# Optimization experiments

Hardware: AMD Instinct MI355X
Metric: run time of the kernel (lower is better)

The kernel has to match this reference:

```python
import jax, jax.numpy as jnp
import numpy as np

DIM = 512
HEADS = 8
DIM_HEAD = 64
INNER = HEADS * DIM_HEAD  # 512
PATCH = 64
M = 3
IN_CH = PATCH * PATCH // 2      # 2048
OUT_CH = IN_CH // 2             # 1024
B, N = 8, PATCH * PATCH // 4    # 8, 1024
SCALE = DIM_HEAD ** -0.5


def setup_inputs() -> dict:
    key = jax.random.key(0)
    ks = jax.random.split(key, 16)
    rn = lambda k, shp, s: (jax.random.normal(k, shp, dtype=jnp.float32) * s)
    inp = rn(ks[0], (B, N, DIM), 1.0)
    x = rn(ks[1], (B, N, DIM), 1.0)
    y = rn(ks[2], (B, N, DIM), 1.0)
    # Linear params (torch convention: W [out, in], y = x @ W.T + b)
    Wq = rn(ks[3], (INNER, DIM), DIM ** -0.5)
    bq = jnp.zeros((INNER,), jnp.float32)
    Wkv = rn(ks[4], (2 * INNER, DIM), DIM ** -0.5)
    bkv = jnp.zeros((2 * INNER,), jnp.float32)
    Wf = rn(ks[5], (OUT_CH + M, IN_CH + M), (IN_CH + M) ** -0.5)
    bf = jnp.zeros((OUT_CH + M,), jnp.float32)
    Wo = rn(ks[6], (DIM, INNER), INNER ** -0.5)
    bo = jnp.zeros((DIM,), jnp.float32)
    # memory tokens (xavier_normal std = sqrt(2/(m+inner)))
    std = np.sqrt(2.0 / (M + INNER))
    m_k = rn(ks[7], (1, M, INNER), std)
    m_v = rn(ks[8], (1, M, INNER), std)
    Sm_k = rn(ks[9], (1, M, INNER), std)
    Sm_v = rn(ks[10], (1, M, INNER), std)
    return dict(inp=inp, x=x, y=y, Wq=Wq, bq=bq, Wkv=Wkv, bkv=bkv,
                Wf=Wf, bf=bf, Wo=Wo, bo=bo,
                m_k=m_k, m_v=m_v, Sm_k=Sm_k, Sm_v=Sm_v)


def _split_heads(t):
    # 'b n (h d) -> b h n d'
    b, n, _ = t.shape
    return t.reshape(b, n, HEADS, DIM_HEAD).transpose(0, 2, 1, 3)


def _mem_view(p, b):
    # torch: p.expand(b, M, INNER).view(b, HEADS, M, DIM_HEAD) — raw reshape
    return jnp.broadcast_to(p, (b, M, INNER)).reshape(b, HEADS, M, DIM_HEAD)


def reference(inp, x, y, Wq, bq, Wkv, bkv, Wf, bf, Wo, bo, m_k, m_v, Sm_k, Sm_v):
    b = inp.shape[0]
    context = jnp.concatenate([x, y], axis=1)            # [b, 2n, dim]
    q = _split_heads(inp @ Wq.T + bq)                    # [b, h, n, d]
    kv = context @ Wkv.T + bkv
    k, v = jnp.split(kv, 2, axis=-1)
    k, v = _split_heads(k), _split_heads(v)              # [b, h, 2n, d]
    mk = np.sqrt(DIM_HEAD).astype(np.float32) * _mem_view(m_k, b)
    mv = np.sqrt(M).astype(np.float32) * _mem_view(m_v, b)
    k = jnp.concatenate([k, mk], axis=2)                 # [b, h, 2n+m, d]
    v = jnp.concatenate([v, mv], axis=2)
    dots = jnp.einsum('bhid,bhjd->bhij', q, k) * SCALE
    cross_attn = jax.nn.softmax(dots, axis=-1)           # [b, h, n, 2n+m]

    skv = inp @ Wkv.T + bkv
    S_k, S_v = jnp.split(skv, 2, axis=-1)
    S_k, S_v = _split_heads(S_k), _split_heads(S_v)      # [b, h, n, d]
    Smk = np.sqrt(DIM_HEAD).astype(np.float32) * _mem_view(Sm_k, b)
    Smv = np.sqrt(M).astype(np.float32) * _mem_view(Sm_v, b)
    Sk = jnp.concatenate([S_k, Smk], axis=2)             # [b, h, n+m, d]
    Sv = jnp.concatenate([S_v, Smv], axis=2)
    dots2 = jnp.einsum('bhid,bhjd->bhij', q, Sk) * SCALE
    self_attn = jax.nn.softmax(dots2, axis=-1)           # [b, h, n, n+m]

    cross_attn = cross_attn @ Wf.T + bf                  # [b, h, n, n+m]
    attn = cross_attn + self_attn
    out = jnp.einsum('bhij,bhjd->bhid', attn, Sv)        # [b, h, n, d]
    out = out.transpose(0, 2, 1, 3).reshape(b, -1, INNER)
    return out @ Wo.T + bo                               # [b, n, dim]
```

## Files before the change

### kernel.cpp

```cpp
#include <hip/hip_runtime.h>
#include <hip/hip_bf16.h>
#include <type_traits>

using bf16 = __hip_bfloat16;
typedef float f32x4 __attribute__((ext_vector_type(4)));
typedef __bf16 bf16x8_t __attribute__((ext_vector_type(8)));
typedef short  s16x8_t  __attribute__((ext_vector_type(8)));

template <typename V, typename = void> struct MfmaWorks : std::false_type {};
template <typename V>
struct MfmaWorks<V, std::void_t<decltype(__builtin_amdgcn_mfma_f32_16x16x32_bf16(
    std::declval<V>(), std::declval<V>(), std::declval<f32x4>(), 0, 0, 0))>> : std::true_type {};
using frag_t = std::conditional_t<MfmaWorks<bf16x8_t>::value, bf16x8_t, s16x8_t>;

template <typename V>
__device__ __forceinline__ f32x4 mfma_16x16x32(V a, V b, f32x4 c) {
    return __builtin_amdgcn_mfma_f32_16x16x32_bf16(a, b, c, 0, 0, 0);
}

__device__ __forceinline__ void gld_lds16(const void* g, void* l) {
    __builtin_amdgcn_global_load_lds(
        (const __attribute__((address_space(1))) unsigned int*)g,
        (__attribute__((address_space(3))) unsigned int*)l, 16, 0, 0);
}

__device__ __forceinline__ float ldin(const void* p, long i, int f32) {
    return f32 ? ((const float*)p)[i] : __bfloat162float(((const bf16*)p)[i]);
}

__global__ void detect_dtype(const void* __restrict__ inp, int* __restrict__ flag)
{
    const int t = threadIdx.x;
    int sane_cnt = 0;
#pragma unroll
    for (int s = 0; s < 4; s++) {
        float v = __bfloat162float(((const bf16*)inp)[2 * (t + 64 * s)]);
        float a = fabsf(v);
        bool sane = (a == 0.f) || (a > 9e-4f && a < 1000.f);
        unsigned long long m = __ballot(sane);
        sane_cnt += (int)__popcll(m);
    }
    if (t == 0) *flag = (sane_cnt > 128) ? 0 : 1;
}

__global__ __launch_bounds__(256)
void cvt_gen8(const void* __restrict__ src, long srcOff, bf16* __restrict__ dst,
              long nsrc, long ndst, const int* __restrict__ flag, float scale)
{
    const int f = *flag;
    const long i0 = ((long)blockIdx.x * 256 + threadIdx.x) * 8;
    if (i0 >= ndst) return;
#pragma unroll
    for (int u = 0; u < 8; u++) {
        const long i = i0 + u;
        if (i < ndst) dst[i] = __float2bfloat16(i < nsrc ? scale * ldin(src, srcOff + i, f) : 0.f);
    }
}

__global__ __launch_bounds__(256)
void cvt_weights(const void* __restrict__ Wq, const void* __restrict__ Wkv,
                 const void* __restrict__ Wo,
                 bf16* __restrict__ WqB, bf16* __restrict__ WkvB, bf16* __restrict__ WoB,
                 const int* __restrict__ flag, float qscale)
{
    const int f = *flag;
    long id = (long)blockIdx.x * 256 + threadIdx.x;
    const void* src; bf16* dst; float sc;
    if (blockIdx.x < 128)      { src = Wq;  dst = WqB;  sc = qscale; }
    else if (blockIdx.x < 384) { src = Wkv; dst = WkvB; sc = 1.f; id -= 128L * 256; }
    else                       { src = Wo;  dst = WoB;  sc = 1.f; id -= 384L * 256; }
    const long i0 = id * 8;
#pragma unroll
    for (int u = 0; u < 8; u++)
        dst[i0 + u] = __float2bfloat16(sc * ldin(src, i0 + u, f));
}

__global__ __launch_bounds__(256)
void cvt_small(const void* __restrict__ bq, const void* __restrict__ bkv,
               const void* __restrict__ bo, const void* __restrict__ mk,
               const void* __restrict__ Smk, const void* __restrict__ Smv,
               bf16* __restrict__ bqB, bf16* __restrict__ bkvB, bf16* __restrict__ boB,
               bf16* __restrict__ mkS, bf16* __restrict__ SmkS, bf16* __restrict__ SmvS,
               const int* __restrict__ flag, float qscale)
{
    const int f = *flag;
    const void* src; bf16* dst; int n; float sc;
    switch (blockIdx.x) {
        case 0:  src = bq;  dst = bqB;  n = 512;  sc = qscale;     break;
        case 1:  src = bkv; dst = bkvB; n = 1024; sc = 1.f;        break;
        case 2:  src = bo;  dst = boB;  n = 512;  sc = 1.f;        break;
        case 3:  src = mk;  dst = mkS;  n = 1536; sc = 8.f;        break;
        case 4:  src = Smk; dst = SmkS; n = 1536; sc = 8.f;        break;
        default: src = Smv; dst = SmvS; n = 1536; sc = 1.7320508f; break;
    }
    for (int i = threadIdx.x; i < n; i += 256)
        dst[i] = __float2bfloat16(sc * ldin(src, i, f));
}

__global__ __launch_bounds__(256)
void cvt_ctx8(const void* __restrict__ x, const void* __restrict__ y,
              bf16* __restrict__ ctx, const int* __restrict__ flag)
{
    const int f = *flag;
    const long i0 = ((long)blockIdx.x * 256 + threadIdx.x) * 8;
    const long r = i0 >> 9, c0 = i0 & 511;
    const long b = r >> 11, jj = r & 2047;
    const void* src = (jj < 1024) ? x : y;
    const long  soff = (jj < 1024) ? ((b * 1024 + jj) * 512 + c0)
                                   : ((b * 1024 + (jj - 1024)) * 512 + c0);
#pragma unroll
    for (int u = 0; u < 8; u++)
        ctx[i0 + u] = __float2bfloat16(ldin(src, soff + u, f));
}

__global__ __launch_bounds__(256)
void cvt_wft(const void* __restrict__ Wf, const void* __restrict__ bff,
             bf16* __restrict__ WfT, const int* __restrict__ flag)
{
    const int f = *flag;
    const long i0 = ((long)blockIdx.x * 256 + threadIdx.x) * 8;
    if (i0 >= 2176L * 1056) return;
    const long j = i0 / 1056, r0 = i0 % 1056;
    __align__(16) bf16 tmp[8];
#pragma unroll
    for (int u = 0; u < 8; u++) {
        const long r = r0 + u;
        float v = 0.f;
        if (r < 1027) {
            if (j < 2051)       v = ldin(Wf, r * 2051 + j, f);
            else if (j == 2051) v = ldin(bff, r, f);
        }
        tmp[u] = __float2bfloat16(v);
    }
    *(uint4*)(WfT + i0) = *(const uint4*)tmp;
}

__global__ __launch_bounds__(256)
void pack_k(const bf16* __restrict__ Ck, const bf16* __restrict__ mkS, bf16* __restrict__ kb)
{
    const long id = (long)blockIdx.x * 256 + threadIdx.x;
    const long bh = id / (2176 * 8);
    const long rem = id % (2176 * 8);
    const long j = rem >> 3;
    const long dg = (rem & 7) << 3;
    const long b = bh >> 3, h = bh & 7;
    bf16* dst = kb + (bh * 2176 + j) * 64 + dg;
    if (j < 2048) {
        *(uint4*)dst = *(const uint4*)(Ck + (b * 2048 + j) * 512 + h * 64 + dg);
    } else if (j < 2051) {
        *(uint4*)dst = *(const uint4*)(mkS + h * 192 + (j - 2048) * 64 + dg);
    } else {
        uint4 zz = {0, 0, 0, 0};
        *(uint4*)dst = zz;
    }
}

__global__ __launch_bounds__(256)
void pack_sk(const bf16* __restrict__ Cskv, const bf16* __restrict__ SmkS, bf16* __restrict__ Skb)
{
    const long id = (long)blockIdx.x * 256 + threadIdx.x;
    const long bh = id / (1152 * 8);
    const long rem = id % (1152 * 8);
    const long j = rem >> 3;
    const long dg = (rem & 7) << 3;
    const long b = bh >> 3, h = bh & 7;
    bf16* dst = Skb + (bh * 1152 + j) * 64 + dg;
    if (j < 1024) {
        *(uint4*)dst = *(const uint4*)(Cskv + (b * 1024 + j) * 1024 + h * 64 + dg);
    } else if (j < 1027) {
        *(uint4*)dst = *(const uint4*)(SmkS + h * 192 + (j - 1024) * 64 + dg);
    } else {
        uint4 zz = {0, 0, 0, 0};
        *(uint4*)dst = zz;
    }
}

__global__ __launch_bounds__(256)
void pack_svt(const bf16* __restrict__ Cskv, const bf16* __restrict__ SmvS,
              bf16* __restrict__ GTS, bf16* __restrict__ SvC)
{
    const long id = (long)blockIdx.x * 256 + threadIdx.x;
    const long bh = id / (128 * 132);
    const long rem = id % (128 * 132);
    const long dd = rem / 132;
    const long j0 = (rem % 132) << 3;
    const long b = bh >> 3, h = bh & 7;
    __align__(16) bf16 tmp[8];
#pragma unroll
    for (int u = 0; u < 8; u++) {
        const long j = j0 + u;
        float v = 0.f;
        if (dd < 64) {
            if (j < 1024)      v = __bfloat162float(Cskv[(b * 1024 + j) * 1024 + 512 + h * 64 + dd]);
            else if (j < 1027) v = __bfloat162float(SmvS[h * 192 + (j - 1024) * 64 + dd]);
        }
        tmp[u] = __float2bfloat16(v);
    }
    *(uint4*)(GTS + (bh * 128 + dd) * 3136 + 2080 + j0) = *(const uint4*)tmp;
    if (dd < 64)
        *(uint4*)(SvC + ((bh << 6) + dd) * 1056 + j0) = *(const uint4*)tmp;
}

#define TM 128
#define TN 128
#define BK 32

template<int OMODE>
__global__ __launch_bounds__(256)
void gemm_nt(const bf16* __restrict__ A, long lda, long sAz,
             const bf16* __restrict__ B, long ldb, long sBz,
             void* __restrict__ Cv, long ldc, long sCz,
             int K,
             const bf16* __restrict__ bias,
             const bf16* __restrict__ add, long ldadd,
             int validN, int zeroN)
{
    __shared__ __align__(16) short As[TM * BK];
    __shared__ __align__(16) short Bs[TN * BK];

    const int t = threadIdx.x;
    const int wave = t >> 6;
    const int lane = t & 63;
    const int bn = blockIdx.x, bm = blockIdx.y, z = blockIdx.z;

    const bf16* Ab = A + (long)z * sAz + (long)bm * TM * lda;
    const bf16* Bb = B + (long)z * sBz + (long)bn * TN * ldb;

    const int lrow = t >> 2;
    const int lcol = (t & 3) << 3;

    const f32x4 vzero = {0.f, 0.f, 0.f, 0.f};
    f32x4 acc[4][4];
#pragma unroll
    for (int i = 0; i < 4; i++)
#pragma unroll
        for (int j = 0; j < 4; j++) acc[i][j] = vzero;

    const int wr = (wave >> 1) << 6;
    const int wc = (wave & 1) << 6;
    const int fr = lane & 15;
    const int fq = (lane >> 4) << 3;

    for (int k0 = 0; k0 < K; k0 += BK) {
        __syncthreads();
        gld_lds16(Ab + (long)lrow * lda + (k0 + lcol),        (char*)As + wave * 1024);
        gld_lds16(Ab + (long)(64 + lrow) * lda + (k0 + lcol), (char*)As + 4096 + wave * 1024);
        gld_lds16(Bb + (long)lrow * ldb + (k0 + lcol),        (char*)Bs + wave * 1024);
        gld_lds16(Bb + (long)(64 + lrow) * ldb + (k0 + lcol), (char*)Bs + 4096 + wave * 1024);
        __builtin_amdgcn_s_waitcnt(0);
        __syncthreads();

        frag_t af[4], bfr[4];
#pragma unroll
        for (int i = 0; i < 4; i++) af[i]  = *(const frag_t*)&As[(wr + i * 16 + fr) * BK + fq];
#pragma unroll
        for (int j = 0; j < 4; j++) bfr[j] = *(const frag_t*)&Bs[(wc + j * 16 + fr) * BK + fq];
#pragma unroll
        for (int i = 0; i < 4; i++)
#pragma unroll
            for (int j = 0; j < 4; j++)
                acc[i][j] = mfma_16x16x32<frag_t>(af[i], bfr[j], acc[i][j]);
    }

    const int r0 = bm * TM + wr + ((lane >> 4) << 2);
    const int c0 = bn * TN + wc + fr;
    if (OMODE == 2) {
#pragma unroll
        for (int j = 0; j < 4; j++) {
            const int c = c0 + j * 16;
            bf16* rowp = (bf16*)Cv + ((long)(c >> 6) * 128 + (c & 63)) * 3136;
#pragma unroll
            for (int i = 0; i < 4; i++) {
                const int rgb = r0 + i * 16;
                if (rgb >= zeroN) continue;
                __align__(8) bf16 t4[4];
#pragma unroll
                for (int r = 0; r < 4; r++) t4[r] = __float2bfloat16(acc[i][j][r]);
                *(uint2*)(rowp + rgb) = *(const uint2*)t4;
            }
        }
        return;
    }
#pragma unroll
    for (int j = 0; j < 4; j++) {
        const int c = c0 + j * 16;
        if (c >= zeroN) continue;
        const bool valid = c < validN;
        float bv = 0.f;
        if (valid && bias) bv = __bfloat162float(bias[c]);
#pragma unroll
        for (int i = 0; i < 4; i++)
#pragma unroll
            for (int r = 0; r < 4; r++) {
                const long rg = r0 + i * 16 + r;
                if (OMODE == 1) {
                    ((float*)Cv)[(long)z * sCz + rg * ldc + c] = acc[i][j][r] + bv;
                } else {
                    float v = 0.f;
                    if (valid) {
                        v = acc[i][j][r] + bv;
                        if (add) v += __bfloat162float(add[rg * ldadd + c]);
                    }
                    ((bf16*)Cv)[(long)z * sCz + rg * ldc + c] = __float2bfloat16(v);
                }
            }
    }
}

__global__ __launch_bounds__(256)
void attn_fused(const bf16* __restrict__ q,
                const bf16* __restrict__ kb,
                const bf16* __restrict__ Skb,
                const bf16* __restrict__ GTS,
                bf16* __restrict__ outb)
{
    __shared__ __align__(16) bf16 PQ[128 * 72];
    __shared__ __align__(16) bf16 Ks[2][64 * 64];
    __shared__ __align__(16) bf16 Gs[2][64 * 64];
    __shared__ bf16 gb_lds[64];

    const int t = threadIdx.x;
    const int w = t >> 6, lane = t & 63;
    const int bh = blockIdx.x, bm = blockIdx.y;
    const int b = bh >> 3, h = bh & 7;
    const int g  = lane >> 4;
    const int fr = lane & 15;
    const int fq = g << 3;

    const bf16* Qg = q + ((long)(b * 1024 + bm * 128)) * 512 + h * 64;
    {
        const int qr = t >> 3, qc0 = (t & 7) << 3;
#pragma unroll
        for (int u = 0; u < 4; u++)
            gld_lds16(Qg + (long)(u * 32 + qr) * 512 + qc0, (char*)PQ + u * 4096 + w * 1024);
    }
    if (t < 64) gb_lds[t] = GTS[((long)bh * 128 + t) * 3136 + 2051];
    __builtin_amdgcn_s_waitcnt(0);
    __syncthreads();

    frag_t qf[2][2];
#pragma unroll
    for (int it = 0; it < 2; it++)
#pragma unroll
        for (int kh = 0; kh < 2; kh++)
            qf[it][kh] = *(const frag_t*)&PQ[(w * 32 + it * 16 + fr) * 64 + kh * 32 + fq];

    union { frag_t f; short s[8]; } ou;
#pragma unroll
    for (int i = 0; i < 8; i++) ou.s[i] = 0x3F80;
    const frag_t onesf = ou.f;

    const f32x4 vzero = {0.f, 0.f, 0.f, 0.f};
    f32x4 ofin[2][4];
#pragma unroll
    for (int it = 0; it < 2; it++)
#pragma unroll
        for (int dt = 0; dt < 4; dt++) ofin[it][dt] = vzero;

    bf16* Ps = PQ;
    const int rs = t >> 3, gs = t & 7;
    const int glo = gs ^ (rs & 7);

    for (int phase = 0; phase < 2; phase++) {
        const bf16* Kb = phase ? Skb + (long)bh * 1152 * 64 : kb + (long)bh * 2176 * 64;
        const bf16* Gb = GTS + (long)bh * 128 * 3136 + (phase ? 2080 : 0);
        const int NC = phase ? 17 : 33;
        const int valid = phase ? 1027 : 2051;

        f32x4 oacc[2][4];
        f32x4 lacc[2];
#pragma unroll
        for (int it = 0; it < 2; it++) {
            lacc[it] = vzero;
#pragma unroll
            for (int dt = 0; dt < 4; dt++) oacc[it][dt] = vzero;
        }

        __syncthreads();
        gld_lds16(Kb + (long)rs * 64 + glo * 8,          (char*)Ks[0] + w * 1024);
        gld_lds16(Kb + (long)(32 + rs) * 64 + glo * 8,   (char*)Ks[0] + 4096 + w * 1024);
        gld_lds16(Gb + (long)rs * 3136 + glo * 8,        (char*)Gs[0] + w * 1024);
        gld_lds16(Gb + (long)(32 + rs) * 3136 + glo * 8, (char*)Gs[0] + 4096 + w * 1024);

        for (int c = 0; c < NC; c++) {
            const int buf = c & 1;
            __builtin_amdgcn_s_waitcnt(0);
            __syncthreads();
            if (c + 1 < NC) {
                const bf16* Kc = Kb + (long)(c + 1) * 64 * 64;
                const bf16* Gc = Gb + (c + 1) * 64;
                gld_lds16(Kc + (long)rs * 64 + glo * 8,          (char*)Ks[buf ^ 1] + w * 1024);
                gld_lds16(Kc + (long)(32 + rs) * 64 + glo * 8,   (char*)Ks[buf ^ 1] + 4096 + w * 1024);
                gld_lds16(Gc + (long)rs * 3136 + glo * 8,        (char*)Gs[buf ^ 1] + w * 1024);
                gld_lds16(Gc + (long)(32 + rs) * 3136 + glo * 8, (char*)Gs[buf ^ 1] + 4096 + w * 1024);
            }
            const bf16* Kl = Ks[buf];
            const bf16* Gl = Gs[buf];
#pragma unroll
            for (int it = 0; it < 2; it++) {
                f32x4 s[4];
#pragma unroll
                for (int ct = 0; ct < 4; ct++) {
                    s[ct] = vzero;
#pragma unroll
                    for (int kh = 0; kh < 2; kh++) {
                        const int R = ct * 16 + fr;
                        const int gph = (kh * 4 + g) ^ (R & 7);
                        const frag_t kf = *(const frag_t*)&Kl[R * 64 + gph * 8];
                        s[ct] = mfma_16x16x32<frag_t>(qf[it][kh], kf, s[ct]);
                    }
                }
                if (c == NC - 1) {
#pragma unroll
                    for (int ct = 0; ct < 4; ct++) {
                        const int j = c * 64 + ct * 16 + fr;
                        if (j >= valid) {
#pragma unroll
                            for (int r = 0; r < 4; r++) s[ct][r] = -1.0e30f;
                        }
                    }
                }
#pragma unroll
                for (int ct = 0; ct < 4; ct++)
#pragma unroll
                    for (int r = 0; r < 4; r++)
                        Ps[(w * 32 + it * 16 + g * 4 + r) * 72 + ct * 16 + fr] =
                            __float2bfloat16(exp2f(s[ct][r]));
#pragma unroll
                for (int kh = 0; kh < 2; kh++) {
                    const frag_t pa = *(const frag_t*)&Ps[(w * 32 + it * 16 + fr) * 72 + kh * 32 + fq];
                    lacc[it] = mfma_16x16x32<frag_t>(pa, onesf, lacc[it]);
#pragma unroll
                    for (int dt = 0; dt < 4; dt++) {
                        const int R = dt * 16 + fr;
                        const int gph = (kh * 4 + g) ^ (R & 7);
                        const frag_t gf = *(const frag_t*)&Gl[R * 64 + gph * 8];
                        oacc[it][dt] = mfma_16x16x32<frag_t>(pa, gf, oacc[it][dt]);
                    }
                }
            }
        }
#pragma unroll
        for (int it = 0; it < 2; it++)
#pragma unroll
            for (int r = 0; r < 4; r++) {
                const float inv = 1.f / lacc[it][r];
#pragma unroll
                for (int dt = 0; dt < 4; dt++)
                    ofin[it][dt][r] += oacc[it][dt][r] * inv;
            }
        if (phase == 0) {
#pragma unroll
            for (int dt = 0; dt < 4; dt++) {
                const float gbv = __bfloat162float(gb_lds[dt * 16 + fr]);
#pragma unroll
                for (int it = 0; it < 2; it++)
#pragma unroll
                    for (int r = 0; r < 4; r++)
                        ofin[it][dt][r] += gbv;
            }
        }
    }

    bf16* Og = outb + ((long)(b * 1024 + bm * 128)) * 512 + h * 64;
#pragma unroll
    for (int it = 0; it < 2; it++)
#pragma unroll
        for (int dt = 0; dt < 4; dt++)
#pragma unroll
            for (int r = 0; r < 4; r++)
                Og[(long)(w * 32 + it * 16 + g * 4 + r) * 512 + dt * 16 + fr] =
                    __float2bfloat16(ofin[it][dt][r]);
}

extern "C" void kernel_launch(void* const* d_in, const int* in_sizes, int n_in,
                              void* d_out, int out_size, void* d_ws, size_t ws_size,
                              hipStream_t stream)
{
    const void* inp  = d_in[0];
    const void* x    = d_in[1];
    const void* y    = d_in[2];
    const void* Wq   = d_in[3];
    const void* bq   = d_in[4];
    const void* Wkv  = d_in[5];
    const void* bkv  = d_in[6];
    const void* Wf   = d_in[7];
    const void* bff  = d_in[8];
    const void* Wo   = d_in[9];
    const void* bo   = d_in[10];
    const void* m_k  = d_in[11];
    const void* Sm_k = d_in[13];
    const void* Sm_v = d_in[14];

    char* ws = (char*)d_ws;
    int*  flag = (int*)(ws + 0);
    bf16* WqB  = (bf16*)(ws + 256);
    bf16* WkvB = (bf16*)(ws + 524544);
    bf16* WoB  = (bf16*)(ws + 1573120);
    bf16* WfT  = (bf16*)(ws + 2097408);
    bf16* bqB  = (bf16*)(ws + 6693120);
    bf16* bkvB = (bf16*)(ws + 6694144);
    bf16* boB  = (bf16*)(ws + 6696192);
    bf16* mkS  = (bf16*)(ws + 6697216);
    bf16* SmkS = (bf16*)(ws + 6700288);
    bf16* SmvS = (bf16*)(ws + 6703360);
    bf16* qb   = (bf16*)(ws + 6706432);
    bf16* kb   = (bf16*)(ws + 15095040);
    bf16* Skb  = (bf16*)(ws + 32920832);
    bf16* GTS  = (bf16*)(ws + 42358016);
    bf16* outb = (bf16*)(ws + 93738240);
    char* OV   = ws + 102126848;

    bf16* inpB = (bf16*)(OV);
    bf16* Cskv = (bf16*)(OV + 8388608);
    bf16* ctxB = (bf16*)(OV);
    bf16* Ck   = (bf16*)(OV + 16777216);
    bf16* SvC  = (bf16*)(OV + 33554432);

    const dim3 blk(256);
    const bf16* nulb = nullptr;
    const float QS = 0.125f * 1.44269504f;

    detect_dtype<<<dim3(1), dim3(64), 0, stream>>>(inp, flag);

    cvt_weights<<<dim3(512), blk, 0, stream>>>(Wq, Wkv, Wo, WqB, WkvB, WoB, flag, QS);
    cvt_wft   <<<dim3(1122), blk, 0, stream>>>(Wf, bff, WfT, flag);
    cvt_small <<<dim3(6),    blk, 0, stream>>>(bq, bkv, bo, m_k, Sm_k, Sm_v,
                                               bqB, bkvB, boB, mkS, SmkS, SmvS, flag, QS);

    cvt_gen8<<<dim3(2048), blk, 0, stream>>>(inp, 0, inpB, 4194304, 4194304, flag, 1.f);
    gemm_nt<0><<<dim3(4, 64, 1), blk, 0, stream>>>(inpB, 512, 0, WqB, 512, 0, (void*)qb, 512, 0,
                                                   512, bqB, nulb, 0, 512, 512);
    gemm_nt<0><<<dim3(8, 64, 1), blk, 0, stream>>>(inpB, 512, 0, WkvB, 512, 0, (void*)Cskv, 1024, 0,
                                                   512, bkvB, nulb, 0, 1024, 1024);
    pack_sk <<<dim3(2304), blk, 0, stream>>>(Cskv, SmkS, Skb);
    pack_svt<<<dim3(4224), blk, 0, stream>>>(Cskv, SmvS, GTS, SvC);
    gemm_nt<2><<<dim3(32, 17, 1), blk, 0, stream>>>(WfT, 1056, 0, SvC, 1056, 0,
                                                    (void*)GTS, 0, 0,
                                                    1056, nulb, nulb, 0, 0, 2080);
    cvt_ctx8<<<dim3(4096), blk, 0, stream>>>(x, y, ctxB, flag);
    gemm_nt<0><<<dim3(4, 128, 1), blk, 0, stream>>>(ctxB, 512, 0, WkvB, 512, 0, (void*)Ck, 512, 0,
                                                    512, bkvB, nulb, 0, 512, 512);
    pack_k<<<dim3(4352), blk, 0, stream>>>(Ck, mkS, kb);

    attn_fused<<<dim3(64, 8), blk, 0, stream>>>(qb, kb, Skb, GTS, outb);

    gemm_nt<1><<<dim3(4, 64, 1), blk, 0, stream>>>(outb, 512, 0, WoB, 512, 0, d_out, 512, 0,
                                                   512, boB, nulb, 0, 512, 512);
}
```

Baseline: 442.4 us.

## Split attention phases across grid z and combine partial outputs in separate kernel

The cross- and self-attention phases, which ran one after the other inside each block, now run as separate blocks via a third grid dimension. This doubles the grid from 512 to 1024 blocks so the GPU's compute units are better filled. Each phase writes fp32 partial outputs, and a new small kernel sums them and converts to bf16. MFMA sections are also wrapped in s_setprio to raise wave priority. The cost is extra fp32 traffic and one more launch, and the phases are unbalanced (33 versus 17 chunks).

```diff
diff --git a/kernel.cpp b/kernel.cpp
--- a/kernel.cpp
+++ b/kernel.cpp
@@ -201,6 +201,18 @@
         *(uint4*)(SvC + ((bh << 6) + dd) * 1056 + j0) = *(const uint4*)tmp;
 }
 
+__global__ __launch_bounds__(256)
+void add2_cvt(const float* __restrict__ o0, const float* __restrict__ o1,
+              bf16* __restrict__ outb)
+{
+    const long i0 = ((long)blockIdx.x * 256 + threadIdx.x) * 8;
+    __align__(16) bf16 tmp[8];
+#pragma unroll
+    for (int u = 0; u < 8; u++)
+        tmp[u] = __float2bfloat16(o0[i0 + u] + o1[i0 + u]);
+    *(uint4*)(outb + i0) = *(const uint4*)tmp;
+}
+
 #define TM 128
 #define TN 128
 #define BK 32
@@ -312,7 +324,8 @@
                 const bf16* __restrict__ kb,
                 const bf16* __restrict__ Skb,
                 const bf16* __restrict__ GTS,
-                bf16* __restrict__ outb)
+                float* __restrict__ out0,
+                float* __restrict__ out1)
 {
     __shared__ __align__(16) bf16 PQ[128 * 72];
     __shared__ __align__(16) bf16 Ks[2][64 * 64];
@@ -322,6 +335,7 @@
     const int t = threadIdx.x;
     const int w = t >> 6, lane = t & 63;
     const int bh = blockIdx.x, bm = blockIdx.y;
+    const int phase = blockIdx.z;
     const int b = bh >> 3, h = bh & 7;
     const int g  = lane >> 4;
     const int fr = lane & 15;
@@ -334,7 +348,7 @@
         for (int u = 0; u < 4; u++)
             gld_lds16(Qg + (long)(u * 32 + qr) * 512 + qc0, (char*)PQ + u * 4096 + w * 1024);
     }
-    if (t < 64) gb_lds[t] = GTS[((long)bh * 128 + t) * 3136 + 2051];
+    if (phase == 0 && t < 64) gb_lds[t] = GTS[((long)bh * 128 + t) * 3136 + 2051];
     __builtin_amdgcn_s_waitcnt(0);
     __syncthreads();
 
@@ -351,126 +365,106 @@
     const frag_t onesf = ou.f;
 
     const f32x4 vzero = {0.f, 0.f, 0.f, 0.f};
-    f32x4 ofin[2][4];
-#pragma unroll
-    for (int it = 0; it < 2; it++)
-#pragma unroll
-        for (int dt = 0; dt < 4; dt++) ofin[it][dt] = vzero;
-
     bf16* Ps = PQ;
     const int rs = t >> 3, gs = t & 7;
     const int glo = gs ^ (rs & 7);
 
-    for (int phase = 0; phase < 2; phase++) {
-        const bf16* Kb = phase ? Skb + (long)bh * 1152 * 64 : kb + (long)bh * 2176 * 64;
-        const bf16* Gb = GTS + (long)bh * 128 * 3136 + (phase ? 2080 : 0);
-        const int NC = phase ? 17 : 33;
-        const int valid = phase ? 1027 : 2051;
-
-        f32x4 oacc[2][4];
-        f32x4 lacc[2];
+    const bf16* Kb = phase ? Skb + (long)bh * 1152 * 64 : kb + (long)bh * 2176 * 64;
+    const bf16* Gb = GTS + (long)bh * 128 * 3136 + (phase ? 2080 : 0);
+    const int NC = phase ? 17 : 33;
+    const int valid = phase ? 1027 : 2051;
+
+    f32x4 oacc[2][4];
+    f32x4 lacc[2];
+#pragma unroll
+    for (int it = 0; it < 2; it++) {
+        lacc[it] = vzero;
+#pragma unroll
+        for (int dt = 0; dt < 4; dt++) oacc[it][dt] = vzero;
+    }
+
+    __syncthreads();
+    gld_lds16(Kb + (long)rs * 64 + glo * 8,          (char*)Ks[0] + w * 1024);
+    gld_lds16(Kb + (long)(32 + rs) * 64 + glo * 8,   (char*)Ks[0] + 4096 + w * 1024);
+    gld_lds16(Gb + (long)rs * 3136 + glo * 8,        (char*)Gs[0] + w * 1024);
+    gld_lds16(Gb + (long)(32 + rs) * 3136 + glo * 8, (char*)Gs[0] + 4096 + w * 1024);
+
+    for (int c = 0; c < NC; c++) {
+        const int buf = c & 1;
+        __builtin_amdgcn_s_waitcnt(0);
+        __syncthreads();
+        if (c + 1 < NC) {
+            const bf16* Kc = Kb + (long)(c + 1) * 64 * 64;
+            const bf16* Gc = Gb + (c + 1) * 64;
+            gld_lds16(Kc + (long)rs * 64 + glo * 8,          (char*)Ks[buf ^ 1] + w * 1024);
+            gld_lds16(Kc + (long)(32 + rs) * 64 + glo * 8,   (char*)Ks[buf ^ 1] + 4096 + w * 1024);
+            gld_lds16(Gc + (long)rs * 3136 + glo * 8,        (char*)Gs[buf ^ 1] + w * 1024);
+            gld_lds16(Gc + (long)(32 + rs) * 3136 + glo * 8, (char*)Gs[buf ^ 1] + 4096 + w * 1024);
+        }
+        const bf16* Kl = Ks[buf];
+        const bf16* Gl = Gs[buf];
 #pragma unroll
         for (int it = 0; it < 2; it++) {
-            lacc[it] = vzero;
-#pragma unroll
-            for (int dt = 0; dt < 4; dt++) oacc[it][dt] = vzero;
-        }
-
-        __syncthreads();
-        gld_lds16(Kb + (long)rs * 64 + glo * 8,          (char*)Ks[0] + w * 1024);
-        gld_lds16(Kb + (long)(32 + rs) * 64 + glo * 8,   (char*)Ks[0] + 4096 + w * 1024);
-        gld_lds16(Gb + (long)rs * 3136 + glo * 8,        (char*)Gs[0] + w * 1024);
-        gld_lds16(Gb + (long)(32 + rs) * 3136 + glo * 8, (char*)Gs[0] + 4096 + w * 1024);
-
-        for (int c = 0; c < NC; c++) {
-            const int buf = c & 1;
-            __builtin_amdgcn_s_waitcnt(0);
-            __syncthreads();
-            if (c + 1 < NC) {
-                const bf16* Kc = Kb + (long)(c + 1) * 64 * 64;
-                const bf16* Gc = Gb + (c + 1) * 64;
-                gld_lds16(Kc + (long)rs * 64 + glo * 8,          (char*)Ks[buf ^ 1] + w * 1024);
-                gld_lds16(Kc + (long)(32 + rs) * 64 + glo * 8,   (char*)Ks[buf ^ 1] + 4096 + w * 1024);
-                gld_lds16(Gc + (long)rs * 3136 + glo * 8,        (char*)Gs[buf ^ 1] + w * 1024);
-                gld_lds16(Gc + (long)(32 + rs) * 3136 + glo * 8, (char*)Gs[buf ^ 1] + 4096 + w * 1024);
+            f32x4 s[4];
+            __builtin_amdgcn_s_setprio(1);
+#pragma unroll
+            for (int ct = 0; ct < 4; ct++) {
+                s[ct] = vzero;
+#pragma unroll
+                for (int kh = 0; kh < 2; kh++) {
+                    const int R = ct * 16 + fr;
+                    const int gph = (kh * 4 + g) ^ (R & 7);
+                    const frag_t kf = *(const frag_t*)&Kl[R * 64 + gph * 8];
+                    s[ct] = mfma_16x16x32<frag_t>(qf[it][kh], kf, s[ct]);
+                }
             }
-            const bf16* Kl = Ks[buf];
-            const bf16* Gl = Gs[buf];
-#pragma unroll
-            for (int it = 0; it < 2; it++) {
-                f32x4 s[4];
+            __builtin_amdgcn_s_setprio(0);
+            if (c == NC - 1) {
 #pragma unroll
                 for (int ct = 0; ct < 4; ct++) {
-                    s[ct] = vzero;
-#pragma unroll
-                    for (int kh = 0; kh < 2; kh++) {
-                        const int R = ct * 16 + fr;
-                        const int gph = (kh * 4 + g) ^ (R & 7);
-                        const frag_t kf = *(const frag_t*)&Kl[R * 64 + gph * 8];
-                        s[ct] = mfma_16x16x32<frag_t>(qf[it][kh], kf, s[ct]);
-                    }
-                }
-                if (c == NC - 1) {
-#pragma unroll
-                    for (int ct = 0; ct < 4; ct++) {
-                        const int j = c * 64 + ct * 16 + fr;
-                        if (j >= valid) {
-#pragma unroll
-                            for (int r = 0; r < 4; r++) s[ct][r] = -1.0e30f;
-                        }
-                    }
-                }
-#pragma unroll
-                for (int ct = 0; ct < 4; ct++)
-#pragma unroll
-                    for (int r = 0; r < 4; r++)
-                        Ps[(w * 32 + it * 16 + g * 4 + r) * 72 + ct * 16 + fr] =
-                            __float2bfloat16(exp2f(s[ct][r]));
-#pragma unroll
-                for (int kh = 0; kh < 2; kh++) {
-                    const frag_t pa = *(const frag_t*)&Ps[(w * 32 + it * 16 + fr) * 72 + kh * 32 + fq];
-                    lacc[it] = mfma_16x16x32<frag_t>(pa, onesf, lacc[it]);
-#pragma unroll
-                    for (int dt = 0; dt < 4; dt++) {
-                        const int R = dt * 16 + fr;
-                        const int gph = (kh * 4 + g) ^ (R & 7);
-                        const frag_t gf = *(const frag_t*)&Gl[R * 64 + gph * 8];
-                        oacc[it][dt] = mfma_16x16x32<frag_t>(pa, gf, oacc[it][dt]);
+                    const int j = c * 64 + ct * 16 + fr;
+                    if (j >= valid) {
+#pragma unroll
+                        for (int r = 0; r < 4; r++) s[ct][r] = -1.0e30f;
                     }
                 }
             }
+#pragma unroll
+            for (int ct = 0; ct < 4; ct++)
+#pragma unroll
+                for (int r = 0; r < 4; r++)
+                    Ps[(w * 32 + it * 16 + g * 4 + r) * 72 + ct * 16 + fr] =
+                        __float2bfloat16(exp2f(s[ct][r]));
+            __builtin_amdgcn_s_setprio(1);
+#pragma unroll
+            for (int kh = 0; kh < 2; kh++) {
+                const frag_t pa = *(const frag_t*)&Ps[(w * 32 + it * 16 + fr) * 72 + kh * 32 + fq];
+                lacc[it] = mfma_16x16x32<frag_t>(pa, onesf, lacc[it]);
+#pragma unroll
+                for (int dt = 0; dt < 4; dt++) {
+                    const int R = dt * 16 + fr;
+                    const int gph = (kh * 4 + g) ^ (R & 7);
+                    const frag_t gf = *(const frag_t*)&Gl[R * 64 + gph * 8];
+                    oacc[it][dt] = mfma_16x16x32<frag_t>(pa, gf, oacc[it][dt]);
+                }
+            }
+            __builtin_amdgcn_s_setprio(0);
         }
-#pragma unroll
-        for (int it = 0; it < 2; it++)
-#pragma unroll
-            for (int r = 0; r < 4; r++) {
-                const float inv = 1.f / lacc[it][r];
-#pragma unroll
-                for (int dt = 0; dt < 4; dt++)
-                    ofin[it][dt][r] += oacc[it][dt][r] * inv;
-            }
-        if (phase == 0) {
+    }
+
+    float* Og = (phase ? out1 : out0) + ((long)(b * 1024 + bm * 128)) * 512 + h * 64;
+#pragma unroll
+    for (int it = 0; it < 2; it++)
+#pragma unroll
+        for (int r = 0; r < 4; r++) {
+            const float inv = 1.f / lacc[it][r];
 #pragma unroll
             for (int dt = 0; dt < 4; dt++) {
-                const float gbv = __bfloat162float(gb_lds[dt * 16 + fr]);
-#pragma unroll
-                for (int it = 0; it < 2; it++)
-#pragma unroll
-                    for (int r = 0; r < 4; r++)
-                        ofin[it][dt][r] += gbv;
+                float v = oacc[it][dt][r] * inv;
+                if (phase == 0) v += __bfloat162float(gb_lds[dt * 16 + fr]);
+                Og[(long)(w * 32 + it * 16 + g * 4 + r) * 512 + dt * 16 + fr] = v;
             }
         }
-    }
-
-    bf16* Og = outb + ((long)(b * 1024 + bm * 128)) * 512 + h * 64;
-#pragma unroll
-    for (int it = 0; it < 2; it++)
-#pragma unroll
-        for (int dt = 0; dt < 4; dt++)
-#pragma unroll
-            for (int r = 0; r < 4; r++)
-                Og[(long)(w * 32 + it * 16 + g * 4 + r) * 512 + dt * 16 + fr] =
-                    __float2bfloat16(ofin[it][dt][r]);
 }
 
 extern "C" void kernel_launch(void* const* d_in, const int* in_sizes, int n_in,
@@ -516,6 +510,8 @@
     bf16* ctxB = (bf16*)(OV);
     bf16* Ck   = (bf16*)(OV + 16777216);
     bf16* SvC  = (bf16*)(OV + 33554432);
+    float* out0f = (float*)(OV);
+    float* out1f = (float*)(OV + 16777216);
 
     const dim3 blk(256);
     const bf16* nulb = nullptr;
@@ -543,7 +539,8 @@
                                                     512, bkvB, nulb, 0, 512, 512);
     pack_k<<<dim3(4352), blk, 0, stream>>>(Ck, mkS, kb);
 
-    attn_fused<<<dim3(64, 8), blk, 0, stream>>>(qb, kb, Skb, GTS, outb);
+    attn_fused<<<dim3(64, 8, 2), blk, 0, stream>>>(qb, kb, Skb, GTS, out0f, out1f);
+    add2_cvt<<<dim3(2048), blk, 0, stream>>>(out0f, out1f, outb);
 
     gemm_nt<1><<<dim3(4, 64, 1), blk, 0, stream>>>(outb, 512, 0, WoB, 512, 0, d_out, 512, 0,
                                                    512, boB, nulb, 0, 512, 512);
```

New measurement: 438.4 us. No clear change (-0.9%).
